# Kernel tuning notes

Measured on AMD Instinct MI355X. Metric: run time of the kernel, lower is better.

## Reference

```python
import jax, jax.numpy as jnp
import numpy as np

THRESH = 1.0   # kwargs_spikes['thresh']
VRESET = 0.0   # kwargs_spikes['vreset'] (not None -> hard reset branch)

@jax.custom_vjp
def rectangle_spike(x):
    # Rectangle surrogate-gradient spike fn: forward heaviside
    return (x >= 0.0).astype(x.dtype)

def _rs_fwd(x):
    return rectangle_spike(x), x

def _rs_bwd(x, g):
    # rectangular surrogate: grad passes where |u - thresh| < 0.5
    return (g * (jnp.abs(x) < 0.5).astype(g.dtype),)

rectangle_spike.defvjp(_rs_fwd, _rs_bwd)

def conv2d(x, w, b):
    # NCHW same-padding conv (padding = kernel_size // 2 with k=3 == SAME)
    y = jax.lax.conv_general_dilated(x, w, (1, 1), 'SAME',
                                     dimension_numbers=('NCHW', 'OIHW', 'NCHW'))
    return y + b[None, :, None, None]

def setup_inputs() -> dict:
    key = jax.random.key(0)
    ks = jax.random.split(key, 4)
    B, T, Cin, H, W = 8, 5, 64, 64, 64
    Cout, K = 64, 3
    # event-frame style sparse binary input
    events = (jax.random.uniform(ks[0], (B, T, Cin, H, W)) < 0.3).astype(jnp.float32)
    scale_in = 1.0 / np.sqrt(Cin * K * K)
    w_in = (jax.random.normal(ks[1], (2 * Cout, Cin, K, K)) * scale_in).astype(jnp.float32)
    b_in = jnp.zeros((2 * Cout,), jnp.float32)
    scale_g = 1.0 / np.sqrt(Cout * K * K)
    w_gate = (jax.random.normal(ks[2], (2 * Cout, Cout, K, K)) * scale_g).astype(jnp.float32)
    b_gate = jnp.zeros((2 * Cout,), jnp.float32)
    thresh_decay = jnp.ones((Cout,), jnp.float32) * 0.9
    return {'events': events, 'w_in': w_in, 'b_in': b_in,
            'w_gate': w_gate, 'b_gate': b_gate, 'thresh_decay': thresh_decay}

def reference(events, w_in, b_in, w_gate, b_gate, thresh_decay):
    # events: [B, T, Cin, H, W] -> [T, B, Cin, H, W], time-reversed (index_select with
    # descending indices, as in the torch forward)
    ev = jnp.flip(jnp.swapaxes(events, 0, 1), axis=0)
    T, B, _, H, W = ev.shape
    Cout = thresh_decay.shape[0]
    vmem0 = jnp.zeros((B, Cout, H, W), ev.dtype)
    spike0 = jnp.zeros((B, Cout, H, W), ev.dtype)

    def step(carry, xs):
        vmem, spike_last = carry
        x, t = xs
        # input path and recurrent gate path each emit 2*Cout channels:
        # first half = current injection, second half = gate pre-activation
        cur_in, gate_in = jnp.split(conv2d(x, w_in, b_in), 2, axis=1)
        cur_g, gate_g = jnp.split(conv2d(spike_last, w_gate, b_gate), 2, axis=1)
        gate = jax.nn.sigmoid(gate_in + gate_g)
        current = cur_in + cur_g
        # per-channel decaying threshold: thresh * thresh_decay^t
        thresh_t = THRESH * thresh_decay[None, :, None, None] ** t
        vmem = gate * vmem + current
        spike = rectangle_spike(vmem - thresh_t)
        # vreset is not None -> hard reset to VRESET where spiked
        vmem = vmem * (1.0 - spike) + VRESET * spike
        return (vmem, spike), spike

    _, spikes = jax.lax.scan(step, (vmem0, spike0),
                             (ev, jnp.arange(T, dtype=ev.dtype)))
    # readout='avg': average firing map over time steps  [B, Cout, H, W]
    return jnp.mean(spikes, axis=0)
```

## Files before the change

### kernel.cpp

```cpp
#include <hip/hip_runtime.h>
#include <cmath>


typedef __attribute__((ext_vector_type(4))) int intx4;

#define HW 64
#define TT 5
#define PLANE 4096
#define CSTR 144
#define USIZE (4 * 66 * CSTR)
#define WPL 147456

__global__ __launch_bounds__(256) void prep_w(
    const float* __restrict__ w_in, const float* __restrict__ w_gate,
    const float* __restrict__ b_in, const float* __restrict__ b_gate,
    const float* __restrict__ tdec,
    signed char* __restrict__ Wp, float* __restrict__ tabs)
{
  const int idx = blockIdx.x * 256 + threadIdx.x;
  if (idx < 9216) {
    const int o   = idx & 127;
    const int q   = (idx >> 7) & 3;
    const int ks  = (idx >> 9) & 1;
    const int tap = idx >> 10;
    const int g = o >> 4, i = o & 15;
    const int row = (i >> 3) * 64 + g * 8 + (i & 7);
    int p1[4], p2[4], p3[4], p4[4];
#pragma unroll
    for (int wd = 0; wd < 4; ++wd) {
      int v1 = 0, v2 = 0, v3 = 0, v4 = 0;
#pragma unroll
      for (int jb = 0; jb < 4; ++jb) {
        const int j = wd * 4 + jb;
        const int c = ks * 64 + q * 16 + j;
        const float w = (c < 64) ? w_in[(row * 64 + c) * 9 + tap]
                                 : w_gate[(row * 64 + (c - 64)) * 9 + tap];
        float a1 = fminf(fmaxf(rintf(w * 256.f), -127.f), 127.f);
        float r1 = w * 256.f - a1;
        float a2 = rintf(r1 * 128.f);
        float r2 = r1 * 128.f - a2;
        float a3 = rintf(r2 * 128.f);
        float r3 = r2 * 128.f - a3;
        float a4 = rintf(r3 * 128.f);
        v1 |= ((int)a1 & 255) << (8 * jb);
        v2 |= ((int)a2 & 255) << (8 * jb);
        v3 |= ((int)a3 & 255) << (8 * jb);
        v4 |= ((int)a4 & 255) << (8 * jb);
      }
      p1[wd] = v1; p2[wd] = v2; p3[wd] = v3; p4[wd] = v4;
    }
    intx4* d = (intx4*)(Wp + (size_t)idx * 16);
    d[0]                          = intx4{p1[0], p1[1], p1[2], p1[3]};
    *(intx4*)((char*)d + WPL)     = intx4{p2[0], p2[1], p2[2], p2[3]};
    *(intx4*)((char*)d + 2 * WPL) = intx4{p3[0], p3[1], p3[2], p3[3]};
    *(intx4*)((char*)d + 3 * WPL) = intx4{p4[0], p4[1], p4[2], p4[3]};
  }
  if (idx < 448) {
    if (idx < 128) tabs[idx] = b_in[idx] + b_gate[idx];
    else {
      const int t = (idx - 128) >> 6, co = (idx - 128) & 63;
      tabs[idx] = powf(tdec[co], (float)t);
    }
  }
}

__global__ __launch_bounds__(256) void prep_ev(
    const float* __restrict__ ev, signed char* __restrict__ evb)
{
  const int row  = blockIdx.x * 4 + (threadIdx.x >> 6);
  const int w    = threadIdx.x & 63;
  const int b  = row / (TT * HW);
  const int rm = row % (TT * HW);
  const int tp = rm / HW;
  const int h  = rm % HW;
  const float* src = ev + ((size_t)(b * TT + tp) * 64) * PLANE + h * HW + w;
  signed char* dst = evb + ((size_t)((b * TT + tp) * PLANE + h * HW + w)) * 64;
#pragma unroll
  for (int k = 0; k < 8; ++k) {
    unsigned long long pk = 0;
#pragma unroll
    for (int j = 0; j < 8; ++j)
      pk |= (src[(size_t)(k * 8 + j) * PLANE] != 0.f)
              ? (1ull << (8 * j)) : 0ull;
    *(unsigned long long*)(dst + k * 8) = pk;
  }
}

__global__ __launch_bounds__(1024, 4) void snn_step(
    const signed char* __restrict__ evb,
    const signed char* __restrict__ Wp,
    const float*       __restrict__ tabs,
    float*             __restrict__ vmemC,
    float*             __restrict__ outC,
    const signed char* __restrict__ s_src,
    signed char*       __restrict__ s_dst,
    float*             __restrict__ outF,
    int t)
{
  __shared__ signed char U[USIZE];

  const int tid = threadIdx.x;
  const int b   = blockIdx.x >> 5;
  const int r0  = (blockIdx.x & 31) * 2;

  const int lane = tid & 63;
  const int g    = (tid >> 6) & 7;
  const int hf   = tid >> 9;
  const int ln   = lane & 15;
  const int q    = lane >> 4;

  const int srow = tid >> 8;
  const int scol = (tid >> 2) & 63;
  const int sch  = tid & 3;
  const int sr   = r0 + srow - 1;
  const bool svalid = (sr >= 0) && (sr < HW);

  intx4 st0 = intx4{0,0,0,0}, st1 = intx4{0,0,0,0};
  bool sstore = false;
  if (svalid) {
    if (sch < 2) {
      const signed char* gs = evb
          + ((size_t)((b * TT + (TT - 1 - t)) * PLANE + sr * HW + scol)) * 64
          + sch * 32;
      st0 = *(const intx4*)gs; st1 = *(const intx4*)(gs + 16);
      sstore = true;
    } else if (t > 0) {
      const signed char* gs = s_src
          + ((size_t)((b * HW + sr) * HW + scol)) * 64 + (sch - 2) * 32;
      st0 = *(const intx4*)gs; st1 = *(const intx4*)(gs + 16);
      sstore = true;
    }
  }

  for (int i = tid; i < USIZE / 16; i += 1024) ((intx4*)U)[i] = intx4{0, 0, 0, 0};
  __syncthreads();
  if (sstore) {
    signed char* du = U + (srow * 66 + scol + 1) * CSTR + sch * 32;
    *(intx4*)du        = st0;
    *(intx4*)(du + 16) = st1;
  }
  __syncthreads();

  intx4 acc1[4], acc2[4], acc3[4], acc4[4];
#pragma unroll
  for (int tt = 0; tt < 4; ++tt) {
    acc1[tt] = intx4{0,0,0,0}; acc2[tt] = intx4{0,0,0,0};
    acc3[tt] = intx4{0,0,0,0}; acc4[tt] = intx4{0,0,0,0};
  }

  const int laneB = ln * CSTR + q * 16;
  const signed char* wlane = Wp + q * 2048 + (g * 16 + ln) * 16;

  for (int tap = 0; tap < 9; ++tap) {
    const int kh = (tap * 11) >> 5;
    const int kw = tap - 3 * kh;
#pragma unroll
    for (int ks = 0; ks < 2; ++ks) {
      const signed char* wp = wlane + (tap * 2 + ks) * 8192;
      const intx4 A1 = *(const intx4*)(wp);
      const intx4 A2 = *(const intx4*)(wp + WPL);
      const intx4 A3 = *(const intx4*)(wp + 2 * WPL);
      const intx4 A4 = *(const intx4*)(wp + 3 * WPL);
      const signed char* ub = U + (hf + kh) * (66 * CSTR) + kw * CSTR + ks * 64 + laneB;
#pragma unroll
      for (int tt = 0; tt < 4; ++tt) {
        const intx4 B = *(const intx4*)(ub + tt * (16 * CSTR));
        acc1[tt] = __builtin_amdgcn_mfma_i32_16x16x64_i8(A1, B, acc1[tt], 0, 0, 0);
        acc2[tt] = __builtin_amdgcn_mfma_i32_16x16x64_i8(A2, B, acc2[tt], 0, 0, 0);
        acc3[tt] = __builtin_amdgcn_mfma_i32_16x16x64_i8(A3, B, acc3[tt], 0, 0, 0);
        acc4[tt] = __builtin_amdgcn_mfma_i32_16x16x64_i8(A4, B, acc4[tt], 0, 0, 0);
      }
    }
  }

  const bool t0 = (t == 0), tL = (t == TT - 1);
  const int co0 = g * 8 + (q & 1) * 4;
  float bc[4], bg[4], th[4];
#pragma unroll
  for (int r = 0; r < 4; ++r) {
    bc[r] = tabs[co0 + r];
    bg[r] = tabs[64 + co0 + r];
    th[r] = tabs[128 + t * 64 + co0 + r];
  }
  const int hh = r0 + hf;
  const size_t pxbase = ((size_t)(b * HW + hh) * HW) * 64 + co0;
#pragma unroll
  for (int tt = 0; tt < 4; ++tt) {
    const int col = tt * 16 + ln;
    const size_t o = pxbase + (size_t)col * 64;
    float mine[4];
#pragma unroll
    for (int r = 0; r < 4; ++r)
      mine[r] = fmaf((float)acc1[tt][r], 0x1p-8f,
                fmaf((float)acc2[tt][r], 0x1p-15f,
                fmaf((float)acc3[tt][r], 0x1p-22f,
                     (float)acc4[tt][r] * 0x1p-29f)));
    float other[4];
#pragma unroll
    for (int r = 0; r < 4; ++r) other[r] = __shfl_xor(mine[r], 32, 64);
    if (q < 2) {
      float4 vm4 = t0 ? float4{0.f,0.f,0.f,0.f} : *(const float4*)&vmemC[o];
      float4 oc4 = t0 ? float4{0.f,0.f,0.f,0.f} : *(const float4*)&outC[o];
      uint fm = 0;
#pragma unroll
      for (int r = 0; r < 4; ++r) {
        const float cur  = mine[r] + bc[r];
        const float gp   = other[r] + bg[r];
        const float gate = 1.f / (1.f + expf(-gp));
        const float v    = gate * (&vm4.x)[r] + cur;
        const bool fired = (v >= th[r]);
        (&vm4.x)[r] = fired ? 0.f : v;
        (&oc4.x)[r] += fired ? 1.f : 0.f;
        fm |= fired ? (1u << (8 * r)) : 0u;
      }
      if (!tL) {
        *(float4*)&vmemC[o] = vm4;
        *(float4*)&outC[o]  = oc4;
        *(uint*)&s_dst[o]   = fm;
      } else {
#pragma unroll
        for (int r = 0; r < 4; ++r)
          outF[((size_t)((b * 64 + co0 + r) * HW + hh)) * HW + col]
              = (&oc4.x)[r] * 0.2f;
      }
    }
  }
}

extern "C" void kernel_launch(void* const* d_in, const int* in_sizes, int n_in,
                              void* d_out, int out_size, void* d_ws, size_t ws_size,
                              hipStream_t stream) {
  const float* events = (const float*)d_in[0];
  const float* w_in   = (const float*)d_in[1];
  const float* b_in   = (const float*)d_in[2];
  const float* w_gate = (const float*)d_in[3];
  const float* b_gate = (const float*)d_in[4];
  const float* tdec   = (const float*)d_in[5];
  float* out = (float*)d_out;

  char* base = (char*)d_ws;
  float*       vmemC = (float*)base;
  float*       outC  = (float*)(base + 8388608);
  signed char* sA    = (signed char*)(base + 16777216);
  signed char* sB    = (signed char*)(base + 18874368);
  signed char* evb   = (signed char*)(base + 20971520);
  signed char* Wp    = (signed char*)(base + 31457280);
  float*       tabs  = (float*)(base + 32047104);

  hipLaunchKernelGGL(prep_w,  dim3(36),  dim3(256), 0, stream,
                     w_in, w_gate, b_in, b_gate, tdec, Wp, tabs);
  hipLaunchKernelGGL(prep_ev, dim3(640), dim3(256), 0, stream, events, evb);

  for (int t = 0; t < TT; ++t) {
    const signed char* ssrc = (t & 1) ? sB : sA;
    signed char*       sdst = (t & 1) ? sA : sB;
    hipLaunchKernelGGL(snn_step, dim3(256), dim3(1024), 0, stream,
                       evb, Wp, tabs, vmemC, outC, ssrc, sdst, out, t);
  }
}
```

Before: 234.2 us.

## Fuse pairs of timesteps per launch with halo recompute and merge prep kernels

Each snn_pair launch now runs two recurrent timesteps. It recomputes the first step's spikes on a widened halo of rows into shared memory, so the second step's gate conv can read them without a global round-trip or an extra launch. The two preprocessing kernels are merged into one, and a final kernel handles the last step. This cuts the launch count from seven to four and removes intermediate vmem/spike global traffic, at the cost of redundant halo convolution work (about 4 of 6 rows per block recomputed for step one) and more shared memory.

Result: slower. 774.9 us (+230.8%).

```diff
diff --git a/kernel.cpp b/kernel.cpp
--- a/kernel.cpp
+++ b/kernel.cpp
@@ -8,85 +8,118 @@
 #define TT 5
 #define PLANE 4096
 #define CSTR 144
-#define USIZE (4 * 66 * CSTR)
+#define RSTR (66 * CSTR)
+#define U1SZ (6 * RSTR)
+#define U2SZ (4 * RSTR)
 #define WPL 147456
 
-__global__ __launch_bounds__(256) void prep_w(
+__global__ __launch_bounds__(256) void prep_all(
     const float* __restrict__ w_in, const float* __restrict__ w_gate,
     const float* __restrict__ b_in, const float* __restrict__ b_gate,
-    const float* __restrict__ tdec,
-    signed char* __restrict__ Wp, float* __restrict__ tabs)
+    const float* __restrict__ tdec, const float* __restrict__ ev,
+    signed char* __restrict__ Wp, float* __restrict__ tabs,
+    signed char* __restrict__ evb)
 {
-  const int idx = blockIdx.x * 256 + threadIdx.x;
-  if (idx < 9216) {
-    const int o   = idx & 127;
-    const int q   = (idx >> 7) & 3;
-    const int ks  = (idx >> 9) & 1;
-    const int tap = idx >> 10;
-    const int g = o >> 4, i = o & 15;
-    const int row = (i >> 3) * 64 + g * 8 + (i & 7);
-    int p1[4], p2[4], p3[4], p4[4];
-#pragma unroll
-    for (int wd = 0; wd < 4; ++wd) {
-      int v1 = 0, v2 = 0, v3 = 0, v4 = 0;
-#pragma unroll
-      for (int jb = 0; jb < 4; ++jb) {
-        const int j = wd * 4 + jb;
-        const int c = ks * 64 + q * 16 + j;
-        const float w = (c < 64) ? w_in[(row * 64 + c) * 9 + tap]
-                                 : w_gate[(row * 64 + (c - 64)) * 9 + tap];
-        float a1 = fminf(fmaxf(rintf(w * 256.f), -127.f), 127.f);
-        float r1 = w * 256.f - a1;
-        float a2 = rintf(r1 * 128.f);
-        float r2 = r1 * 128.f - a2;
-        float a3 = rintf(r2 * 128.f);
-        float r3 = r2 * 128.f - a3;
-        float a4 = rintf(r3 * 128.f);
-        v1 |= ((int)a1 & 255) << (8 * jb);
-        v2 |= ((int)a2 & 255) << (8 * jb);
-        v3 |= ((int)a3 & 255) << (8 * jb);
-        v4 |= ((int)a4 & 255) << (8 * jb);
-      }
-      p1[wd] = v1; p2[wd] = v2; p3[wd] = v3; p4[wd] = v4;
-    }
-    intx4* d = (intx4*)(Wp + (size_t)idx * 16);
-    d[0]                          = intx4{p1[0], p1[1], p1[2], p1[3]};
-    *(intx4*)((char*)d + WPL)     = intx4{p2[0], p2[1], p2[2], p2[3]};
-    *(intx4*)((char*)d + 2 * WPL) = intx4{p3[0], p3[1], p3[2], p3[3]};
-    *(intx4*)((char*)d + 3 * WPL) = intx4{p4[0], p4[1], p4[2], p4[3]};
-  }
-  if (idx < 448) {
-    if (idx < 128) tabs[idx] = b_in[idx] + b_gate[idx];
-    else {
-      const int t = (idx - 128) >> 6, co = (idx - 128) & 63;
-      tabs[idx] = powf(tdec[co], (float)t);
-    }
-  }
-}
-
-__global__ __launch_bounds__(256) void prep_ev(
-    const float* __restrict__ ev, signed char* __restrict__ evb)
+  if (blockIdx.x < 36) {
+    const int idx = blockIdx.x * 256 + threadIdx.x;
+    {
+      const int o   = idx & 127;
+      const int q   = (idx >> 7) & 3;
+      const int ks  = (idx >> 9) & 1;
+      const int tap = idx >> 10;
+      const int g = o >> 4, i = o & 15;
+      const int row = (i >> 3) * 64 + g * 8 + (i & 7);
+      int p1[4], p2[4], p3[4], p4[4];
+#pragma unroll
+      for (int wd = 0; wd < 4; ++wd) {
+        int v1 = 0, v2 = 0, v3 = 0, v4 = 0;
+#pragma unroll
+        for (int jb = 0; jb < 4; ++jb) {
+          const int j = wd * 4 + jb;
+          const int c = ks * 64 + q * 16 + j;
+          const float w = (c < 64) ? w_in[(row * 64 + c) * 9 + tap]
+                                   : w_gate[(row * 64 + (c - 64)) * 9 + tap];
+          float a1 = fminf(fmaxf(rintf(w * 256.f), -127.f), 127.f);
+          float r1 = w * 256.f - a1;
+          float a2 = rintf(r1 * 128.f);
+          float r2 = r1 * 128.f - a2;
+          float a3 = rintf(r2 * 128.f);
+          float r3 = r2 * 128.f - a3;
+          float a4 = rintf(r3 * 128.f);
+          v1 |= ((int)a1 & 255) << (8 * jb);
+          v2 |= ((int)a2 & 255) << (8 * jb);
+          v3 |= ((int)a3 & 255) << (8 * jb);
+          v4 |= ((int)a4 & 255) << (8 * jb);
+        }
+        p1[wd] = v1; p2[wd] = v2; p3[wd] = v3; p4[wd] = v4;
+      }
+      intx4* d = (intx4*)(Wp + (size_t)idx * 16);
+      d[0]                          = intx4{p1[0], p1[1], p1[2], p1[3]};
+      *(intx4*)((char*)d + WPL)     = intx4{p2[0], p2[1], p2[2], p2[3]};
+      *(intx4*)((char*)d + 2 * WPL) = intx4{p3[0], p3[1], p3[2], p3[3]};
+      *(intx4*)((char*)d + 3 * WPL) = intx4{p4[0], p4[1], p4[2], p4[3]};
+    }
+    if (idx < 448) {
+      if (idx < 128) tabs[idx] = b_in[idx] + b_gate[idx];
+      else {
+        const int t = (idx - 128) >> 6, co = (idx - 128) & 63;
+        tabs[idx] = powf(tdec[co], (float)t);
+      }
+    }
+  } else {
+    const int row = (blockIdx.x - 36) * 4 + (threadIdx.x >> 6);
+    const int w   = threadIdx.x & 63;
+    const int b  = row / (TT * HW);
+    const int rm = row % (TT * HW);
+    const int tp = rm / HW;
+    const int h  = rm % HW;
+    const float* src = ev + ((size_t)(b * TT + tp) * 64) * PLANE + h * HW + w;
+    signed char* dst = evb + ((size_t)((b * TT + tp) * PLANE + h * HW + w)) * 64;
+#pragma unroll
+    for (int k = 0; k < 8; ++k) {
+      unsigned long long pk = 0;
+#pragma unroll
+      for (int j = 0; j < 8; ++j)
+        pk |= (src[(size_t)(k * 8 + j) * PLANE] != 0.f) ? (1ull << (8 * j)) : 0ull;
+      *(unsigned long long*)(dst + k * 8) = pk;
+    }
+  }
+}
+
+__device__ __forceinline__ void conv128(const signed char* __restrict__ Ub, int lr,
+    int laneB, const signed char* __restrict__ wlane,
+    intx4* __restrict__ a1, intx4* __restrict__ a2,
+    intx4* __restrict__ a3, intx4* __restrict__ a4)
 {
-  const int row  = blockIdx.x * 4 + (threadIdx.x >> 6);
-  const int w    = threadIdx.x & 63;
-  const int b  = row / (TT * HW);
-  const int rm = row % (TT * HW);
-  const int tp = rm / HW;
-  const int h  = rm % HW;
-  const float* src = ev + ((size_t)(b * TT + tp) * 64) * PLANE + h * HW + w;
-  signed char* dst = evb + ((size_t)((b * TT + tp) * PLANE + h * HW + w)) * 64;
-#pragma unroll
-  for (int k = 0; k < 8; ++k) {
-    unsigned long long pk = 0;
-#pragma unroll
-    for (int j = 0; j < 8; ++j)
-      pk |= (src[(size_t)(k * 8 + j) * PLANE] != 0.f)
-              ? (1ull << (8 * j)) : 0ull;
-    *(unsigned long long*)(dst + k * 8) = pk;
-  }
-}
-
-__global__ __launch_bounds__(1024, 4) void snn_step(
+  for (int tap = 0; tap < 9; ++tap) {
+    const int kh = (tap * 11) >> 5;
+    const int kw = tap - 3 * kh;
+#pragma unroll
+    for (int ks = 0; ks < 2; ++ks) {
+      const signed char* wp = wlane + (tap * 2 + ks) * 8192;
+      const intx4 A1 = *(const intx4*)(wp);
+      const intx4 A2 = *(const intx4*)(wp + WPL);
+      const intx4 A3 = *(const intx4*)(wp + 2 * WPL);
+      const intx4 A4 = *(const intx4*)(wp + 3 * WPL);
+      const signed char* ub = Ub + (lr - 1 + kh) * RSTR + kw * CSTR + ks * 64 + laneB;
+#pragma unroll
+      for (int tt = 0; tt < 4; ++tt) {
+        const intx4 B = *(const intx4*)(ub + tt * (16 * CSTR));
+        a1[tt] = __builtin_amdgcn_mfma_i32_16x16x64_i8(A1, B, a1[tt], 0, 0, 0);
+        a2[tt] = __builtin_amdgcn_mfma_i32_16x16x64_i8(A2, B, a2[tt], 0, 0, 0);
+        a3[tt] = __builtin_amdgcn_mfma_i32_16x16x64_i8(A3, B, a3[tt], 0, 0, 0);
+        a4[tt] = __builtin_amdgcn_mfma_i32_16x16x64_i8(A4, B, a4[tt], 0, 0, 0);
+      }
+    }
+  }
+}
+
+__device__ __forceinline__ float recon(int a1, int a2, int a3, int a4) {
+  return fmaf((float)a1, 0x1p-8f, fmaf((float)a2, 0x1p-15f,
+         fmaf((float)a3, 0x1p-22f, (float)a4 * 0x1p-29f)));
+}
+
+__global__ __launch_bounds__(1024, 4) void snn_pair(
     const signed char* __restrict__ evb,
     const signed char* __restrict__ Wp,
     const float*       __restrict__ tabs,
@@ -94,10 +127,10 @@
     float*             __restrict__ outC,
     const signed char* __restrict__ s_src,
     signed char*       __restrict__ s_dst,
-    float*             __restrict__ outF,
     int t)
 {
-  __shared__ signed char U[USIZE];
+  __shared__ signed char U1[U1SZ];
+  __shared__ signed char U2[U2SZ];
 
   const int tid = threadIdx.x;
   const int b   = blockIdx.x >> 5;
@@ -109,99 +142,226 @@
   const int ln   = lane & 15;
   const int q    = lane >> 4;
 
+  for (int i = tid; i < U1SZ / 16; i += 1024) ((intx4*)U1)[i] = intx4{0,0,0,0};
+  for (int i = tid; i < U2SZ / 16; i += 1024) ((intx4*)U2)[i] = intx4{0,0,0,0};
+  __syncthreads();
+
+  const int pe1 = TT - 1 - t, pe2 = TT - 2 - t;
+  for (int i = tid; i < 2048; i += 1024) {
+    if (i < 1536) {
+      const bool sp = (i >= 768);
+      const int  j  = sp ? (i - 768) : i;
+      const int half = j & 1;
+      const int px   = j >> 1;
+      const int lr   = px >> 6;
+      const int col  = px & 63;
+      const int row  = r0 - 2 + lr;
+      if (row >= 0 && row < HW && (!sp || t > 0)) {
+        const signed char* src = sp
+          ? s_src + ((size_t)((b * HW + row) * HW + col)) * 64 + half * 32
+          : evb + ((size_t)((b * TT + pe1) * PLANE + row * HW + col)) * 64 + half * 32;
+        signed char* dst = U1 + (lr * 66 + col + 1) * CSTR + (sp ? 64 : 0) + half * 32;
+        *(intx4*)dst        = *(const intx4*)src;
+        *(intx4*)(dst + 16) = *(const intx4*)(src + 16);
+      }
+    } else {
+      const int j = i - 1536;
+      const int half = j & 1;
+      const int px   = j >> 1;
+      const int lr   = px >> 6;
+      const int col  = px & 63;
+      const int row  = r0 - 1 + lr;
+      if (row >= 0 && row < HW) {
+        const signed char* src =
+          evb + ((size_t)((b * TT + pe2) * PLANE + row * HW + col)) * 64 + half * 32;
+        signed char* dst = U2 + (lr * 66 + col + 1) * CSTR + half * 32;
+        *(intx4*)dst        = *(const intx4*)src;
+        *(intx4*)(dst + 16) = *(const intx4*)(src + 16);
+      }
+    }
+  }
+  __syncthreads();
+
+  const int laneB = ln * CSTR + q * 16;
+  const signed char* wlane = Wp + q * 2048 + (g * 16 + ln) * 16;
+  const int co0 = g * 8 + (q & 1) * 4;
+  float bc[4], bg[4];
+#pragma unroll
+  for (int r = 0; r < 4; ++r) { bc[r] = tabs[co0 + r]; bg[r] = tabs[64 + co0 + r]; }
+
+  float vmreg[4][4];
+  uint  cnt_t[4];
+
+#pragma unroll 1
+  for (int hr = 0; hr < 2; ++hr) {
+    const int rr = hr ? (r0 + 1 - hf) : (hf ? r0 + 2 : r0 - 1);
+    const int lr = rr - (r0 - 2);
+    intx4 a1[4], a2[4], a3[4], a4[4];
+#pragma unroll
+    for (int tt = 0; tt < 4; ++tt) {
+      a1[tt] = intx4{0,0,0,0}; a2[tt] = intx4{0,0,0,0};
+      a3[tt] = intx4{0,0,0,0}; a4[tt] = intx4{0,0,0,0};
+    }
+    conv128(U1, lr, laneB, wlane, a1, a2, a3, a4);
+
+    const bool inr = (rr >= 0) && (rr < HW);
+    const int lr2 = rr - (r0 - 1);
+#pragma unroll
+    for (int tt = 0; tt < 4; ++tt) {
+      const int col = tt * 16 + ln;
+      float mine[4], other[4];
+#pragma unroll
+      for (int r = 0; r < 4; ++r)
+        mine[r] = recon(a1[tt][r], a2[tt][r], a3[tt][r], a4[tt][r]);
+#pragma unroll
+      for (int r = 0; r < 4; ++r) other[r] = __shfl_xor(mine[r], 32, 64);
+      if (q < 2 && inr) {
+        float4 vm4 = float4{0.f, 0.f, 0.f, 0.f};
+        if (t > 0)
+          vm4 = *(const float4*)&vmemC[((size_t)((b * HW + rr) * HW + col)) * 64 + co0];
+        uint fm = 0;
+#pragma unroll
+        for (int r = 0; r < 4; ++r) {
+          const float cur  = mine[r] + bc[r];
+          const float gp   = other[r] + bg[r];
+          const float gate = 1.f / (1.f + expf(-gp));
+          const float v    = gate * (&vm4.x)[r] + cur;
+          const bool fired = (v >= tabs[128 + t * 64 + co0 + r]);
+          (&vm4.x)[r] = fired ? 0.f : v;
+          fm |= fired ? (1u << (8 * r)) : 0u;
+        }
+        if (hr) {
+#pragma unroll
+          for (int r = 0; r < 4; ++r) vmreg[tt][r] = (&vm4.x)[r];
+          cnt_t[tt] = fm;
+        }
+        *(uint*)(U2 + (lr2 * 66 + col + 1) * CSTR + 64 + co0) = fm;
+      }
+    }
+  }
+  __syncthreads();
+
+  {
+    const int rr = r0 + 1 - hf;
+    const int lr = 2 - hf;
+    intx4 a1[4], a2[4], a3[4], a4[4];
+#pragma unroll
+    for (int tt = 0; tt < 4; ++tt) {
+      a1[tt] = intx4{0,0,0,0}; a2[tt] = intx4{0,0,0,0};
+      a3[tt] = intx4{0,0,0,0}; a4[tt] = intx4{0,0,0,0};
+    }
+    conv128(U2, lr, laneB, wlane, a1, a2, a3, a4);
+#pragma unroll
+    for (int tt = 0; tt < 4; ++tt) {
+      const int col = tt * 16 + ln;
+      float mine[4], other[4];
+#pragma unroll
+      for (int r = 0; r < 4; ++r)
+        mine[r] = recon(a1[tt][r], a2[tt][r], a3[tt][r], a4[tt][r]);
+#pragma unroll
+      for (int r = 0; r < 4; ++r) other[r] = __shfl_xor(mine[r], 32, 64);
+      if (q < 2) {
+        float4 vm4; float4 c4;
+        uint fm = 0;
+#pragma unroll
+        for (int r = 0; r < 4; ++r) {
+          const float cur  = mine[r] + bc[r];
+          const float gp   = other[r] + bg[r];
+          const float gate = 1.f / (1.f + expf(-gp));
+          const float v    = gate * vmreg[tt][r] + cur;
+          const bool fired = (v >= tabs[128 + (t + 1) * 64 + co0 + r]);
+          (&vm4.x)[r] = fired ? 0.f : v;
+          fm |= fired ? (1u << (8 * r)) : 0u;
+          (&c4.x)[r] = (float)((cnt_t[tt] >> (8 * r)) & 255u)
+                     + (fired ? 1.f : 0.f);
+        }
+        const size_t o = ((size_t)((b * HW + rr) * HW + col)) * 64 + co0;
+        *(float4*)&vmemC[o] = vm4;
+        *(uint*)&s_dst[o]   = fm;
+        if (t == 0) {
+          *(float4*)&outC[o] = c4;
+        } else {
+          const float4 p = *(const float4*)&outC[o];
+          *(float4*)&outC[o] = float4{p.x + c4.x, p.y + c4.y, p.z + c4.z, p.w + c4.w};
+        }
+      }
+    }
+  }
+}
+
+__global__ __launch_bounds__(1024, 4) void snn_final(
+    const signed char* __restrict__ evb,
+    const signed char* __restrict__ Wp,
+    const float*       __restrict__ tabs,
+    const float*       __restrict__ vmemC,
+    const float*       __restrict__ outC,
+    const signed char* __restrict__ s_src,
+    float*             __restrict__ outF)
+{
+  __shared__ signed char U[U2SZ];
+
+  const int tid = threadIdx.x;
+  const int b   = blockIdx.x >> 5;
+  const int r0  = (blockIdx.x & 31) * 2;
+
+  const int lane = tid & 63;
+  const int g    = (tid >> 6) & 7;
+  const int hf   = tid >> 9;
+  const int ln   = lane & 15;
+  const int q    = lane >> 4;
+
   const int srow = tid >> 8;
   const int scol = (tid >> 2) & 63;
   const int sch  = tid & 3;
   const int sr   = r0 + srow - 1;
   const bool svalid = (sr >= 0) && (sr < HW);
-
   intx4 st0 = intx4{0,0,0,0}, st1 = intx4{0,0,0,0};
-  bool sstore = false;
   if (svalid) {
-    if (sch < 2) {
-      const signed char* gs = evb
-          + ((size_t)((b * TT + (TT - 1 - t)) * PLANE + sr * HW + scol)) * 64
-          + sch * 32;
-      st0 = *(const intx4*)gs; st1 = *(const intx4*)(gs + 16);
-      sstore = true;
-    } else if (t > 0) {
-      const signed char* gs = s_src
-          + ((size_t)((b * HW + sr) * HW + scol)) * 64 + (sch - 2) * 32;
-      st0 = *(const intx4*)gs; st1 = *(const intx4*)(gs + 16);
-      sstore = true;
-    }
-  }
-
-  for (int i = tid; i < USIZE / 16; i += 1024) ((intx4*)U)[i] = intx4{0, 0, 0, 0};
+    const signed char* gs = (sch < 2)
+      ? evb + ((size_t)((b * TT + 0) * PLANE + sr * HW + scol)) * 64 + sch * 32
+      : s_src + ((size_t)((b * HW + sr) * HW + scol)) * 64 + (sch - 2) * 32;
+    st0 = *(const intx4*)gs; st1 = *(const intx4*)(gs + 16);
+  }
+  for (int i = tid; i < U2SZ / 16; i += 1024) ((intx4*)U)[i] = intx4{0,0,0,0};
   __syncthreads();
-  if (sstore) {
+  if (svalid) {
     signed char* du = U + (srow * 66 + scol + 1) * CSTR + sch * 32;
-    *(intx4*)du        = st0;
-    *(intx4*)(du + 16) = st1;
+    *(intx4*)du = st0; *(intx4*)(du + 16) = st1;
   }
   __syncthreads();
-
-  intx4 acc1[4], acc2[4], acc3[4], acc4[4];
-#pragma unroll
-  for (int tt = 0; tt < 4; ++tt) {
-    acc1[tt] = intx4{0,0,0,0}; acc2[tt] = intx4{0,0,0,0};
-    acc3[tt] = intx4{0,0,0,0}; acc4[tt] = intx4{0,0,0,0};
-  }
 
   const int laneB = ln * CSTR + q * 16;
   const signed char* wlane = Wp + q * 2048 + (g * 16 + ln) * 16;
-
-  for (int tap = 0; tap < 9; ++tap) {
-    const int kh = (tap * 11) >> 5;
-    const int kw = tap - 3 * kh;
-#pragma unroll
-    for (int ks = 0; ks < 2; ++ks) {
-      const signed char* wp = wlane + (tap * 2 + ks) * 8192;
-      const intx4 A1 = *(const intx4*)(wp);
-      const intx4 A2 = *(const intx4*)(wp + WPL);
-      const intx4 A3 = *(const intx4*)(wp + 2 * WPL);
-      const intx4 A4 = *(const intx4*)(wp + 3 * WPL);
-      const signed char* ub = U + (hf + kh) * (66 * CSTR) + kw * CSTR + ks * 64 + laneB;
-#pragma unroll
-      for (int tt = 0; tt < 4; ++tt) {
-        const intx4 B = *(const intx4*)(ub + tt * (16 * CSTR));
-        acc1[tt] = __builtin_amdgcn_mfma_i32_16x16x64_i8(A1, B, acc1[tt], 0, 0, 0);
-        acc2[tt] = __builtin_amdgcn_mfma_i32_16x16x64_i8(A2, B, acc2[tt], 0, 0, 0);
-        acc3[tt] = __builtin_amdgcn_mfma_i32_16x16x64_i8(A3, B, acc3[tt], 0, 0, 0);
-        acc4[tt] = __builtin_amdgcn_mfma_i32_16x16x64_i8(A4, B, acc4[tt], 0, 0, 0);
-      }
-    }
-  }
-
-  const bool t0 = (t == 0), tL = (t == TT - 1);
+  intx4 a1[4], a2[4], a3[4], a4[4];
+#pragma unroll
+  for (int tt = 0; tt < 4; ++tt) {
+    a1[tt] = intx4{0,0,0,0}; a2[tt] = intx4{0,0,0,0};
+    a3[tt] = intx4{0,0,0,0}; a4[tt] = intx4{0,0,0,0};
+  }
+  conv128(U, 1 + hf, laneB, wlane, a1, a2, a3, a4);
+
   const int co0 = g * 8 + (q & 1) * 4;
   float bc[4], bg[4], th[4];
 #pragma unroll
   for (int r = 0; r < 4; ++r) {
     bc[r] = tabs[co0 + r];
     bg[r] = tabs[64 + co0 + r];
-    th[r] = tabs[128 + t * 64 + co0 + r];
+    th[r] = tabs[128 + 4 * 64 + co0 + r];
   }
   const int hh = r0 + hf;
-  const size_t pxbase = ((size_t)(b * HW + hh) * HW) * 64 + co0;
 #pragma unroll
   for (int tt = 0; tt < 4; ++tt) {
     const int col = tt * 16 + ln;
-    const size_t o = pxbase + (size_t)col * 64;
-    float mine[4];
+    float mine[4], other[4];
 #pragma unroll
     for (int r = 0; r < 4; ++r)
-      mine[r] = fmaf((float)acc1[tt][r], 0x1p-8f,
-                fmaf((float)acc2[tt][r], 0x1p-15f,
-                fmaf((float)acc3[tt][r], 0x1p-22f,
-                     (float)acc4[tt][r] * 0x1p-29f)));
-    float other[4];
+      mine[r] = recon(a1[tt][r], a2[tt][r], a3[tt][r], a4[tt][r]);
 #pragma unroll
     for (int r = 0; r < 4; ++r) other[r] = __shfl_xor(mine[r], 32, 64);
     if (q < 2) {
-      float4 vm4 = t0 ? float4{0.f,0.f,0.f,0.f} : *(const float4*)&vmemC[o];
-      float4 oc4 = t0 ? float4{0.f,0.f,0.f,0.f} : *(const float4*)&outC[o];
-      uint fm = 0;
+      const size_t o = ((size_t)((b * HW + hh) * HW + col)) * 64 + co0;
+      const float4 vm4 = *(const float4*)&vmemC[o];
+      const float4 oc4 = *(const float4*)&outC[o];
 #pragma unroll
       for (int r = 0; r < 4; ++r) {
         const float cur  = mine[r] + bc[r];
@@ -209,19 +369,8 @@
         const float gate = 1.f / (1.f + expf(-gp));
         const float v    = gate * (&vm4.x)[r] + cur;
         const bool fired = (v >= th[r]);
-        (&vm4.x)[r] = fired ? 0.f : v;
-        (&oc4.x)[r] += fired ? 1.f : 0.f;
-        fm |= fired ? (1u << (8 * r)) : 0u;
-      }
-      if (!tL) {
-        *(float4*)&vmemC[o] = vm4;
-        *(float4*)&outC[o]  = oc4;
-        *(uint*)&s_dst[o]   = fm;
-      } else {
-#pragma unroll
-        for (int r = 0; r < 4; ++r)
-          outF[((size_t)((b * 64 + co0 + r) * HW + hh)) * HW + col]
-              = (&oc4.x)[r] * 0.2f;
+        outF[((size_t)((b * 64 + co0 + r) * HW + hh)) * HW + col]
+            = ((&oc4.x)[r] + (fired ? 1.f : 0.f)) * 0.2f;
       }
     }
   }
@@ -241,20 +390,19 @@
   char* base = (char*)d_ws;
   float*       vmemC = (float*)base;
   float*       outC  = (float*)(base + 8388608);
-  signed char* sA    = (signed char*)(base + 16777216);
-  signed char* sB    = (signed char*)(base + 18874368);
+  signed char* s1    = (signed char*)(base + 16777216);
+  signed char* s3    = (signed char*)(base + 18874368);
   signed char* evb   = (signed char*)(base + 20971520);
   signed char* Wp    = (signed char*)(base + 31457280);
   float*       tabs  = (float*)(base + 32047104);
 
-  hipLaunchKernelGGL(prep_w,  dim3(36),  dim3(256), 0, stream,
-                     w_in, w_gate, b_in, b_gate, tdec, Wp, tabs);
-  hipLaunchKernelGGL(prep_ev, dim3(640), dim3(256), 0, stream, events, evb);
-
-  for (int t = 0; t < TT; ++t) {
-    const signed char* ssrc = (t & 1) ? sB : sA;
-    signed char*       sdst = (t & 1) ? sA : sB;
-    hipLaunchKernelGGL(snn_step, dim3(256), dim3(1024), 0, stream,
-                       evb, Wp, tabs, vmemC, outC, ssrc, sdst, out, t);
-  }
-}
+  hipLaunchKernelGGL(prep_all, dim3(676), dim3(256), 0, stream,
+                     w_in, w_gate, b_in, b_gate, tdec, events, Wp, tabs, evb);
+
+  hipLaunchKernelGGL(snn_pair, dim3(256), dim3(1024), 0, stream,
+                     evb, Wp, tabs, vmemC, outC, s1 , s1, 0);
+  hipLaunchKernelGGL(snn_pair, dim3(256), dim3(1024), 0, stream,
+                     evb, Wp, tabs, vmemC, outC, s1, s3, 2);
+  hipLaunchKernelGGL(snn_final, dim3(256), dim3(1024), 0, stream,
+                     evb, Wp, tabs, vmemC, outC, s3, out);
+}
```
